# Optimization experiments

Measured on AMD Instinct MI355X. Metric: run time of the kernel, lower is better.

## Reference

```python
import jax, jax.numpy as jnp
import numpy as np

# Grid / problem sizes (match init_kwargs)
B, D, H, W = 2, 64, 256, 256      # batch + spatial_shape
N = 524288                         # active voxels
IN_DIM, HID = 32, 32               # input_dim, hidden_dim
C_IN = IN_DIM + HID                # conv in-channels (64)
C_OUT = 4 * HID                    # conv out-channels (128)
OFFSETS = [(dz, dy, dx) for dz in (-1, 0, 1) for dy in (-1, 0, 1) for dx in (-1, 0, 1)]


def setup_inputs() -> dict:
    key = jax.random.key(0)
    ks = jax.random.split(key, 5)
    # Unique active-voxel coordinates: odd multiplier is a bijection mod 2^k grid size.
    total = B * D * H * W
    MULT = 2654435761  # odd => injective on arange(N) mod total (total is a power of 2)
    lin = (np.arange(N, dtype=np.int64) * MULT) % total
    b = lin // (D * H * W)
    r = lin % (D * H * W)
    z = r // (H * W)
    r = r % (H * W)
    y = r // W
    x = r % W
    coors = jnp.asarray(np.stack([b, z, y, x], axis=1).astype(np.int32))  # [N,4]
    x_features = jax.random.normal(ks[0], (N, IN_DIM), jnp.float32)
    h_features = jax.random.normal(ks[1], (N, HID), jnp.float32)
    c_features = jax.random.normal(ks[2], (N, HID), jnp.float32)
    weight = jax.random.normal(ks[3], (27, C_IN, C_OUT), jnp.float32) * 0.05
    bias = jax.random.normal(ks[4], (C_OUT,), jnp.float32) * 0.05
    return {"x_features": x_features, "h_features": h_features,
            "c_features": c_features, "weight": weight, "bias": bias,
            "coors": coors, "batch_size": B}


def _subm_conv3d(feats, weight, bias, coors):
    """Submanifold sparse 3x3x3 conv: output only at active sites;
    gather-GEMM-scatter via a dense coordinate->point-id map (the rulebook)."""
    b, z, y, x = coors[:, 0], coors[:, 1], coors[:, 2], coors[:, 3]
    pid = jnp.arange(N, dtype=jnp.int32)
    idx_map = jnp.full((B, D, H, W), -1, jnp.int32).at[b, z, y, x].set(pid)
    out = jnp.zeros((N, C_OUT), feats.dtype) + bias  # [N, 4*HID]
    for k, (dz, dy, dx) in enumerate(OFFSETS):
        nz, ny, nx = z + dz, y + dy, x + dx
        inb = (nz >= 0) & (nz < D) & (ny >= 0) & (ny < H) & (nx >= 0) & (nx < W)
        nid = idx_map[b, jnp.clip(nz, 0, D - 1), jnp.clip(ny, 0, H - 1), jnp.clip(nx, 0, W - 1)]
        nid = jnp.where(inb, nid, -1)
        valid = nid >= 0
        gathered = jnp.where(valid[:, None], feats[jnp.maximum(nid, 0)], 0.0)  # [N, C_IN]
        out = out + gathered @ weight[k]
    return out


def reference(x_features, h_features, c_features, weight, bias, coors, batch_size):
    combined = jnp.concatenate([x_features, h_features], axis=1)  # [N, C_IN]
    cc = _subm_conv3d(combined, weight, bias, coors)              # [N, 4*HID]
    cc_i, cc_f, cc_o, cc_g = jnp.split(cc, 4, axis=1)
    i = jax.nn.sigmoid(cc_i)
    f = jax.nn.sigmoid(cc_f)
    o = jax.nn.sigmoid(cc_o)
    g = jnp.tanh(cc_g)
    c_next = f * c_features + i * g
    h_next = o * jnp.tanh(c_next)
    return (h_next, c_next)
```

## Files before the change

### kernel.cpp

```cpp
#include <hip/hip_runtime.h>
#include <stdint.h>

#define N_PTS 524288
#define DQ 64
#define HQ 256
#define WQ 256
#define MAP_BYTES (2*DQ*HQ*WQ*4)
#define NBKT 4096

typedef short bf8  __attribute__((ext_vector_type(8)));
typedef float f16v __attribute__((ext_vector_type(16)));

static __device__ __forceinline__ short f2bf(float f) {
    union { float f; uint32_t u; } v; v.f = f;
    return (short)((v.u + 0x7fffu + ((v.u >> 16) & 1u)) >> 16);
}
static __device__ __forceinline__ float fast_sigmoid(float x) {
    return 1.f / (1.f + __expf(-x));
}
static __device__ __forceinline__ float fast_tanh(float x) {
    return 1.f - 2.f / (__expf(2.f * x) + 1.f);
}

__global__ void k_hist(const int* __restrict__ coors, int* __restrict__ hist) {
    int n = blockIdx.x * 256 + threadIdx.x;
    int4 c = ((const int4*)coors)[n];
    int mbase = ((c.x*DQ + c.y)*HQ + c.z)*WQ + c.w;
    atomicAdd(&hist[mbase >> 11], 1);
}

__global__ void k_scan(int* __restrict__ hist) {
    __shared__ int wsum[4];
    int tid = threadIdx.x;
    int lane = tid & 63, wv = tid >> 6;
    int v[16]; int s = 0;
    #pragma unroll
    for (int i = 0; i < 16; i++) { v[i] = hist[tid*16 + i]; s += v[i]; }
    int sc = s;
    #pragma unroll
    for (int d = 1; d < 64; d <<= 1) {
        int t = __shfl_up(sc, d, 64);
        if (lane >= d) sc += t;
    }
    if (lane == 63) wsum[wv] = sc;
    __syncthreads();
    int base = 0;
    #pragma unroll
    for (int w = 0; w < 4; w++) if (w < wv) base += wsum[w];
    int excl = base + sc - s;
    #pragma unroll
    for (int i = 0; i < 16; i++) { int c = v[i]; hist[tid*16 + i] = excl; excl += c; }
}

__global__ void k_rank(const int* __restrict__ coors, int* __restrict__ hist,
                       int* __restrict__ rank, int* __restrict__ sorg) {
    int n = blockIdx.x * 256 + threadIdx.x;
    int4 c = ((const int4*)coors)[n];
    int mbase = ((c.x*DQ + c.y)*HQ + c.z)*WQ + c.w;
    int slot = atomicAdd(&hist[mbase >> 11], 1);
    rank[n] = slot;
    sorg[slot] = n;
}

__global__ void k_feats(const float* __restrict__ xf, const float* __restrict__ hf,
                        const int* __restrict__ coors, const int* __restrict__ rank,
                        short* __restrict__ fb, int* __restrict__ map,
                        int4* __restrict__ rcoors) {
    int t = blockIdx.x * 256 + threadIdx.x;
    int n = t >> 3, seg = t & 7;
    int r = rank[n];
    const float* src = (seg < 4) ? (xf + n*32 + seg*8) : (hf + n*32 + seg*8 - 32);
    float4 a = ((const float4*)src)[0];
    float4 b = ((const float4*)src)[1];
    bf8 rv;
    rv[0]=f2bf(a.x); rv[1]=f2bf(a.y); rv[2]=f2bf(a.z); rv[3]=f2bf(a.w);
    rv[4]=f2bf(b.x); rv[5]=f2bf(b.y); rv[6]=f2bf(b.z); rv[7]=f2bf(b.w);
    ((bf8*)fb)[r*8 + seg] = rv;
    if (seg == 0) {
        int4 c = ((const int4*)coors)[n];
        map[((c.x*DQ + c.y)*HQ + c.z)*WQ + c.w] = r;
        rcoors[r] = c;
    }
}

__global__ void k_wt(const float* __restrict__ w, short* __restrict__ wt) {
    int t = blockIdx.x * 256 + threadIdx.x;
    if (t >= 27*64*128) return;
    int jj = t & 7, c = (t >> 3) & 127, jg = (t >> 10) & 7, k = t >> 13;
    int j = jg*8 + jj;
    wt[t] = f2bf(w[(k*64 + j)*128 + c]);
}

__launch_bounds__(256, 2)
__global__ void k_main(const int* __restrict__ map, const short* __restrict__ fb,
                       const short* __restrict__ wt, const float* __restrict__ bias,
                       const float* __restrict__ cfeat, const int4* __restrict__ rcoors,
                       const int* __restrict__ sorg, const short* __restrict__ zp,
                       float* __restrict__ out)
{
    __shared__ short Wlds[2][8192];

    const int tid  = threadIdx.x;
    const int lane = tid & 63;
    const int wv   = tid >> 6;
    const int l31  = lane & 31;
    const int lhi  = lane >> 5;

    const int bid   = (blockIdx.x & 7) * 256 + (blockIdx.x >> 3);
    const int pbase = bid * 256;
    const int p     = pbase + wv*64 + lane;

    const int4 cr = rcoors[p];
    const int mbase = ((cr.x*DQ + cr.y)*HQ + cr.z)*WQ + cr.w;

    auto probe = [&](int ko) -> int {
        int dz = ko/9 - 1, dy = (ko/3)%3 - 1, dxo = ko%3 - 1;
        if ((unsigned)(cr.y + dz) < (unsigned)DQ &&
            (unsigned)(cr.z + dy) < (unsigned)HQ &&
            (unsigned)(cr.w + dxo) < (unsigned)WQ)
            return map[mbase + (dz*HQ + dy)*WQ + dxo];
        return -1;
    };

    auto stageW = [&](int ko) {
        const short* src = wt + ko*8192;
        #pragma unroll
        for (int i = 0; i < 4; i++) {
            int cb = i*256 + wv*64;
            __builtin_amdgcn_global_load_lds(
                (const __attribute__((address_space(1))) void*)(src + (size_t)(cb + lane)*8),
                (__attribute__((address_space(3))) void*)&Wlds[ko & 1][cb*8],
                16, 0, 0);
        }
    };

    auto gather = [&](int n0, int n1, bf8* dst) {
        const short* s0 = (n0 >= 0) ? (fb + (size_t)n0*64 + lhi*8) : (zp + lhi*8);
        const short* s1 = (n1 >= 0) ? (fb + (size_t)n1*64 + lhi*8) : (zp + lhi*8);
        #pragma unroll
        for (int j = 0; j < 4; j++) {
            dst[j]     = *(const bf8*)(s0 + j*16);
            dst[4 + j] = *(const bf8*)(s1 + j*16);
        }
    };

    f16v acc[2][4];
    #pragma unroll
    for (int mt = 0; mt < 2; mt++)
        #pragma unroll
        for (int ct = 0; ct < 4; ct++) {
            float bv = bias[ct*32 + l31];
            #pragma unroll
            for (int r = 0; r < 16; r++) acc[mt][ct][r] = bv;
        }

    int pA = probe(0);
    int pB = probe(1);
    int pr_old = probe(2);
    stageW(0);

    bf8 a_cur[8], a_next[8];
    {
        int g0 = __shfl(pA, l31, 64);
        int g1 = __shfl(pA, l31 + 32, 64);
        gather(g0, g1, a_cur);
    }
    int g0n = __shfl(pB, l31, 64);
    int g1n = __shfl(pB, l31 + 32, 64);

    #pragma unroll 1
    for (int ko = 0; ko < 27; ko++) {
        __syncthreads();

        if (ko < 26) {
            stageW(ko + 1);
            gather(g0n, g1n, a_next);
        }
        int pr_new = (ko < 24) ? probe(ko + 3) : -1;

        const int buf = ko & 1;
        #pragma unroll
        for (int ks = 0; ks < 4; ks++) {
            int jg = ks*2 + lhi;
            const short* wb = &Wlds[buf][(jg*128 + l31)*8];
            #pragma unroll
            for (int ct = 0; ct < 4; ct++) {
                bf8 b = *(const bf8*)(wb + ct*32*8);
                acc[0][ct] = __builtin_amdgcn_mfma_f32_32x32x16_bf16(a_cur[ks],     b, acc[0][ct], 0, 0, 0);
                acc[1][ct] = __builtin_amdgcn_mfma_f32_32x32x16_bf16(a_cur[4 + ks], b, acc[1][ct], 0, 0, 0);
            }
        }

        if (ko < 25) {
            g0n = __shfl(pr_old, l31, 64);
            g1n = __shfl(pr_old, l31 + 32, 64);
            pr_old = pr_new;
        }
        #pragma unroll
        for (int j = 0; j < 8; j++) a_cur[j] = a_next[j];
    }

    #pragma unroll
    for (int mt = 0; mt < 2; mt++) {
        #pragma unroll
        for (int r = 0; r < 16; r++) {
            int row = (r & 3) + 8*(r >> 2) + 4*lhi;
            int pp  = pbase + wv*64 + mt*32 + row;
            int orig = sorg[pp];
            float gi = acc[mt][0][r];
            float gf = acc[mt][1][r];
            float go = acc[mt][2][r];
            float gg = acc[mt][3][r];
            float cv = cfeat[orig*32 + l31];
            float si = fast_sigmoid(gi);
            float sf = fast_sigmoid(gf);
            float so = fast_sigmoid(go);
            float tg = fast_tanh(gg);
            float cn = sf*cv + si*tg;
            float hn = so * fast_tanh(cn);
            out[orig*32 + l31] = hn;
            out[N_PTS*32 + orig*32 + l31] = cn;
        }
    }
}

extern "C" void kernel_launch(void* const* d_in, const int* in_sizes, int n_in,
                              void* d_out, int out_size, void* d_ws, size_t ws_size,
                              hipStream_t stream) {
    const float* xf    = (const float*)d_in[0];
    const float* hf    = (const float*)d_in[1];
    const float* cf    = (const float*)d_in[2];
    const float* w     = (const float*)d_in[3];
    const float* bias  = (const float*)d_in[4];
    const int*   coors = (const int*)d_in[5];
    float* out = (float*)d_out;

    char* base = (char*)d_ws;
    int*   map    = (int*)base;
    short* fb     = (short*)(base + MAP_BYTES);
    short* wtb    = (short*)(base + MAP_BYTES + (size_t)N_PTS*64*2);
    short* zp     = (short*)(base + 100663296 + 442368);
    int*   rank   = (int*)(base + 101106176);
    int*   sorg   = (int*)(base + 103203328);
    int4*  rcoors = (int4*)(base + 105300480);
    int*   hist   = (int*)(base + 113689088);

    hipMemsetAsync(map, 0xFF, MAP_BYTES, stream);
    hipMemsetAsync(hist, 0, NBKT*4, stream);
    hipMemsetAsync(zp, 0, 256, stream);
    k_hist<<<N_PTS/256, 256, 0, stream>>>(coors, hist);
    k_scan<<<1, 256, 0, stream>>>(hist);
    k_rank<<<N_PTS/256, 256, 0, stream>>>(coors, hist, rank, sorg);
    k_feats<<<(N_PTS*8)/256, 256, 0, stream>>>(xf, hf, coors, rank, fb, map, rcoors);
    k_wt<<<(27*64*128 + 255)/256, 256, 0, stream>>>(w, wtb);
    k_main<<<N_PTS/256, 256, 0, stream>>>(map, fb, wtb, bias, cf, rcoors, sorg, zp, out);
}
```

Measured before the change: 581.1 us.

## Fuse rank into feats kernel, drop rcoors buffer and LDS weight staging

The bucket-rank atomic is folded into the feature-conversion kernel, with the slot broadcast across the 8 lanes of each point by a shuffle. This removes one kernel launch, the rank array and the rcoors array. The main kernel now reads coordinates through sorg, and it reads weights straight from global memory (relying on L1/L2) instead of double-buffering them into LDS with a barrier every offset. This cuts the per-iteration __syncthreads and the LDS traffic. In exchange, each wave issues redundant global weight loads that may contend with the feature gathers, and coordinate reads become indirect.

```diff
diff --git a/kernel.cpp b/kernel.cpp
--- a/kernel.cpp
+++ b/kernel.cpp
@@ -52,35 +52,29 @@
     for (int i = 0; i < 16; i++) { int c = v[i]; hist[tid*16 + i] = excl; excl += c; }
 }
 
-__global__ void k_rank(const int* __restrict__ coors, int* __restrict__ hist,
-                       int* __restrict__ rank, int* __restrict__ sorg) {
-    int n = blockIdx.x * 256 + threadIdx.x;
-    int4 c = ((const int4*)coors)[n];
-    int mbase = ((c.x*DQ + c.y)*HQ + c.z)*WQ + c.w;
-    int slot = atomicAdd(&hist[mbase >> 11], 1);
-    rank[n] = slot;
-    sorg[slot] = n;
-}
-
 __global__ void k_feats(const float* __restrict__ xf, const float* __restrict__ hf,
-                        const int* __restrict__ coors, const int* __restrict__ rank,
+                        const int* __restrict__ coors, int* __restrict__ hist,
                         short* __restrict__ fb, int* __restrict__ map,
-                        int4* __restrict__ rcoors) {
+                        int* __restrict__ sorg) {
     int t = blockIdx.x * 256 + threadIdx.x;
     int n = t >> 3, seg = t & 7;
-    int r = rank[n];
+    int lane = threadIdx.x & 63;
+    int slot = 0;
+    if (seg == 0) {
+        int4 c = ((const int4*)coors)[n];
+        int mb = ((c.x*DQ + c.y)*HQ + c.z)*WQ + c.w;
+        slot = atomicAdd(&hist[mb >> 11], 1);
+        map[mb] = slot;
+        sorg[slot] = n;
+    }
+    slot = __shfl(slot, lane & 56, 64);
     const float* src = (seg < 4) ? (xf + n*32 + seg*8) : (hf + n*32 + seg*8 - 32);
     float4 a = ((const float4*)src)[0];
     float4 b = ((const float4*)src)[1];
     bf8 rv;
     rv[0]=f2bf(a.x); rv[1]=f2bf(a.y); rv[2]=f2bf(a.z); rv[3]=f2bf(a.w);
     rv[4]=f2bf(b.x); rv[5]=f2bf(b.y); rv[6]=f2bf(b.z); rv[7]=f2bf(b.w);
-    ((bf8*)fb)[r*8 + seg] = rv;
-    if (seg == 0) {
-        int4 c = ((const int4*)coors)[n];
-        map[((c.x*DQ + c.y)*HQ + c.z)*WQ + c.w] = r;
-        rcoors[r] = c;
-    }
+    ((bf8*)fb)[slot*8 + seg] = rv;
 }
 
 __global__ void k_wt(const float* __restrict__ w, short* __restrict__ wt) {
@@ -94,12 +88,10 @@
 __launch_bounds__(256, 2)
 __global__ void k_main(const int* __restrict__ map, const short* __restrict__ fb,
                        const short* __restrict__ wt, const float* __restrict__ bias,
-                       const float* __restrict__ cfeat, const int4* __restrict__ rcoors,
+                       const float* __restrict__ cfeat, const int* __restrict__ coors,
                        const int* __restrict__ sorg, const short* __restrict__ zp,
                        float* __restrict__ out)
 {
-    __shared__ short Wlds[2][8192];
-
     const int tid  = threadIdx.x;
     const int lane = tid & 63;
     const int wv   = tid >> 6;
@@ -110,7 +102,8 @@
     const int pbase = bid * 256;
     const int p     = pbase + wv*64 + lane;
 
-    const int4 cr = rcoors[p];
+    const int orig = sorg[p];
+    const int4 cr = ((const int4*)coors)[orig];
     const int mbase = ((cr.x*DQ + cr.y)*HQ + cr.z)*WQ + cr.w;
 
     auto probe = [&](int ko) -> int {
@@ -122,18 +115,6 @@
         return -1;
     };
 
-    auto stageW = [&](int ko) {
-        const short* src = wt + ko*8192;
-        #pragma unroll
-        for (int i = 0; i < 4; i++) {
-            int cb = i*256 + wv*64;
-            __builtin_amdgcn_global_load_lds(
-                (const __attribute__((address_space(1))) void*)(src + (size_t)(cb + lane)*8),
-                (__attribute__((address_space(3))) void*)&Wlds[ko & 1][cb*8],
-                16, 0, 0);
-        }
-    };
-
     auto gather = [&](int n0, int n1, bf8* dst) {
         const short* s0 = (n0 >= 0) ? (fb + (size_t)n0*64 + lhi*8) : (zp + lhi*8);
         const short* s1 = (n1 >= 0) ? (fb + (size_t)n1*64 + lhi*8) : (zp + lhi*8);
@@ -157,7 +138,6 @@
     int pA = probe(0);
     int pB = probe(1);
     int pr_old = probe(2);
-    stageW(0);
 
     bf8 a_cur[8], a_next[8];
     {
@@ -170,19 +150,14 @@
 
     #pragma unroll 1
     for (int ko = 0; ko < 27; ko++) {
-        __syncthreads();
-
-        if (ko < 26) {
-            stageW(ko + 1);
-            gather(g0n, g1n, a_next);
-        }
+        if (ko < 26) gather(g0n, g1n, a_next);
         int pr_new = (ko < 24) ? probe(ko + 3) : -1;
 
-        const int buf = ko & 1;
+        const short* wko = wt + ko*8192;
         #pragma unroll
         for (int ks = 0; ks < 4; ks++) {
             int jg = ks*2 + lhi;
-            const short* wb = &Wlds[buf][(jg*128 + l31)*8];
+            const short* wb = wko + (jg*128 + l31)*8;
             #pragma unroll
             for (int ct = 0; ct < 4; ct++) {
                 bf8 b = *(const bf8*)(wb + ct*32*8);
@@ -206,20 +181,20 @@
         for (int r = 0; r < 16; r++) {
             int row = (r & 3) + 8*(r >> 2) + 4*lhi;
             int pp  = pbase + wv*64 + mt*32 + row;
-            int orig = sorg[pp];
+            int opp = sorg[pp];
             float gi = acc[mt][0][r];
             float gf = acc[mt][1][r];
             float go = acc[mt][2][r];
             float gg = acc[mt][3][r];
-            float cv = cfeat[orig*32 + l31];
+            float cv = cfeat[opp*32 + l31];
             float si = fast_sigmoid(gi);
             float sf = fast_sigmoid(gf);
             float so = fast_sigmoid(go);
             float tg = fast_tanh(gg);
             float cn = sf*cv + si*tg;
             float hn = so * fast_tanh(cn);
-            out[orig*32 + l31] = hn;
-            out[N_PTS*32 + orig*32 + l31] = cn;
+            out[opp*32 + l31] = hn;
+            out[N_PTS*32 + opp*32 + l31] = cn;
         }
     }
 }
@@ -238,20 +213,17 @@
     char* base = (char*)d_ws;
     int*   map    = (int*)base;
     short* fb     = (short*)(base + MAP_BYTES);
-    short* wtb    = (short*)(base + MAP_BYTES + (size_t)N_PTS*64*2);
-    short* zp     = (short*)(base + 100663296 + 442368);
-    int*   rank   = (int*)(base + 101106176);
-    int*   sorg   = (int*)(base + 103203328);
-    int4*  rcoors = (int4*)(base + 105300480);
-    int*   hist   = (int*)(base + 113689088);
+    short* wtb    = (short*)(base + 100663296);
+    short* zp     = (short*)(base + 101105664);
+    int*   sorg   = (int*)(base + 101106176);
+    int*   hist   = (int*)(base + 103203328);
 
     hipMemsetAsync(map, 0xFF, MAP_BYTES, stream);
     hipMemsetAsync(hist, 0, NBKT*4, stream);
     hipMemsetAsync(zp, 0, 256, stream);
     k_hist<<<N_PTS/256, 256, 0, stream>>>(coors, hist);
     k_scan<<<1, 256, 0, stream>>>(hist);
-    k_rank<<<N_PTS/256, 256, 0, stream>>>(coors, hist, rank, sorg);
-    k_feats<<<(N_PTS*8)/256, 256, 0, stream>>>(xf, hf, coors, rank, fb, map, rcoors);
+    k_feats<<<(N_PTS*8)/256, 256, 0, stream>>>(xf, hf, coors, hist, fb, map, sorg);
     k_wt<<<(27*64*128 + 255)/256, 256, 0, stream>>>(w, wtb);
-    k_main<<<N_PTS/256, 256, 0, stream>>>(map, fb, wtb, bias, cf, rcoors, sorg, zp, out);
-}
+    k_main<<<N_PTS/256, 256, 0, stream>>>(map, fb, wtb, bias, cf, coors, sorg, zp, out);
+}
```

Result: slower. 669.6 us (+15.2%).
